# Optimization experiments

Hardware: AMD Instinct MI355X
Metric: run time of the kernel (lower is better)

The kernel has to match this reference:

```python
import jax, jax.numpy as jnp
import numpy as np

B, S, D, H = 4, 2048, 512, 8
DH = D // H  # depth per head = 64


def setup_inputs() -> dict:
    key = jax.random.key(0)
    ks = jax.random.split(key, 8)
    scale = 1.0 / np.sqrt(D)
    return {
        "query": jax.random.normal(ks[0], (B, S, D), jnp.float32),
        "key": jax.random.normal(ks[1], (B, S, D), jnp.float32),
        "value": jax.random.normal(ks[2], (B, S, D), jnp.float32),
        "mask": jax.random.randint(ks[3], (B, S), 0, 2, jnp.int32),
        "wq_w": jax.random.normal(ks[4], (D, D), jnp.float32) * scale,
        "wq_b": jnp.zeros((D,), jnp.float32),
        "wk_w": jax.random.normal(ks[5], (D, D), jnp.float32) * scale,
        "wk_b": jnp.zeros((D,), jnp.float32),
        "wv_w": jax.random.normal(ks[6], (D, D), jnp.float32) * scale,
        "wv_b": jnp.zeros((D,), jnp.float32),
        "wo_w": jax.random.normal(ks[7], (D, D), jnp.float32) * scale,
        "wo_b": jnp.zeros((D,), jnp.float32),
    }


def _split_heads(x):
    # [B, S, D] -> [B, H, S, DH]
    b, s, _ = x.shape
    return x.reshape(b, s, H, DH).transpose(0, 2, 1, 3)


def reference(query, key, value, mask, wq_w, wq_b, wk_w, wk_b, wv_w, wv_b, wo_w, wo_b):
    q = _split_heads(query @ wq_w + wq_b)   # [B,H,S,DH]
    k = _split_heads(key @ wk_w + wk_b)
    v = _split_heads(value @ wv_w + wv_b)

    scale = 1.0 / jnp.sqrt(jnp.asarray(DH, jnp.float32))
    logits = jnp.einsum('bhqd,bhkd->bhqk', q, k) * scale  # [B,H,S,S]
    # additive key-padding mask: 1 -> masked (adds -1e9)
    m = mask.astype(logits.dtype)[:, None, None, :]  # [B,1,1,S]
    logits = logits + m * -1e9
    weights = jax.nn.softmax(logits, axis=-1)
    attn = jnp.einsum('bhqk,bhkd->bhqd', weights, v)  # [B,H,S,DH]
    attn = attn.transpose(0, 2, 1, 3).reshape(query.shape[0], -1, D)  # [B,S,D]
    return attn @ wo_w + wo_b
```

## Files before the change

kernel.cpp:

```cpp
#include <hip/hip_runtime.h>
#include <stdint.h>

#define QSCALE (0.125f * 1.44269504088896340736f)
#define MASKNEG (-1.442695e9f)

typedef unsigned short u16;
typedef unsigned int u32;
typedef __bf16 bf16x8 __attribute__((ext_vector_type(8)));
typedef float f32x4 __attribute__((ext_vector_type(4)));
typedef float f32x16 __attribute__((ext_vector_type(16)));
typedef u16 u16x8 __attribute__((ext_vector_type(8)));
typedef u32 u32x4 __attribute__((ext_vector_type(4)));

__device__ __forceinline__ u16 f2bf(float f) {
  u32 u = __float_as_uint(f);
  u += 0x7fffu + ((u >> 16) & 1u);
  return (u16)(u >> 16);
}

__device__ __forceinline__ u32 cvtpk(float lo, float hi) {
  u32 d;
  asm("v_cvt_pk_bf16_f32 %0, %1, %2" : "=v"(d) : "v"(lo), "v"(hi));
  return d;
}

__device__ __forceinline__ void plswap(u32& a, u32& b) {
  asm("v_permlane32_swap_b32 %0, %1" : "+v"(a), "+v"(b));
}

__device__ __forceinline__ void gload16(const void* src, void* ldsbase) {
  __builtin_amdgcn_global_load_lds(
      (const __attribute__((address_space(1))) u32*)src,
      (__attribute__((address_space(3))) u32*)ldsbase, 16, 0, 0);
}

__device__ __forceinline__ u16x8 pack8(const float4& a, const float4& b) {
  u32x4 w;
  w[0] = cvtpk(a.x, a.y);
  w[1] = cvtpk(a.z, a.w);
  w[2] = cvtpk(b.x, b.y);
  w[3] = cvtpk(b.z, b.w);
  return __builtin_bit_cast(u16x8, w);
}

#define QKV_BAR(N)                                           \
  do {                                                       \
    asm volatile("s_waitcnt vmcnt(" #N ")" ::: "memory");    \
    asm volatile("s_waitcnt lgkmcnt(0)" ::: "memory");       \
    __builtin_amdgcn_sched_barrier(0);                       \
    __builtin_amdgcn_s_barrier();                            \
  } while (0)

__global__ __launch_bounds__(256) void conv_w(const float* __restrict__ wq,
                                              const float* __restrict__ wk,
                                              const float* __restrict__ wv,
                                              const float* __restrict__ wo,
                                              u16* __restrict__ wT) {
  const float* src = (blockIdx.z == 0) ? wq : (blockIdx.z == 1) ? wk
                    : (blockIdx.z == 2) ? wv : wo;
  u16* dst = wT + (size_t)blockIdx.z * 262144;
  __shared__ float t[64][65];
  const int n0 = blockIdx.x * 64, k0 = blockIdx.y * 64;
  const int lr = threadIdx.x >> 6, lc = threadIdx.x & 63;
#pragma unroll
  for (int it = 0; it < 16; ++it) {
    const int row = it * 4 + lr;
    t[row][lc] = src[(size_t)(k0 + row) * 512 + n0 + lc];
  }
  __syncthreads();
#pragma unroll
  for (int it = 0; it < 16; ++it) {
    const int row = it * 4 + lr;
    dst[(size_t)(n0 + row) * 512 + k0 + lc] = f2bf(t[lc][row]);
  }
}

__global__ __launch_bounds__(256, 2) void gemm_qkv(
    const float* __restrict__ xqf, const float* __restrict__ xkf,
    const float* __restrict__ xvf, const u16* __restrict__ wT,
    const float* __restrict__ bq, const float* __restrict__ bk,
    const float* __restrict__ bv, u16* __restrict__ qws, u16* __restrict__ kws,
    u16* __restrict__ vTw) {
  __shared__ __align__(16) char lds[65536];
  const int hw = blockIdx.x;
  const int lg = (hw & 7) * 96 + (hw >> 3);
  const int z = lg >> 8;
  const int rem = lg & 255;
  const int m0 = (rem >> 2) * 128, n0 = (rem & 3) * 128;
  const float* A = (z == 0) ? xqf : (z == 1) ? xkf : xvf;
  const u16* Bt = wT + (size_t)z * 262144;
  const float* bias = (z == 0) ? bq : (z == 1) ? bk : bv;

  const int tid = threadIdx.x;
  const int lane = tid & 63;
  const int wave = tid >> 6;
  const int wm = wave >> 1, wn = wave & 1;
  const int srow = tid >> 3;
  const int sc16 = tid & 7;

  f32x4 acc[4][4] = {};
  float4 s0[8], s1[8];

  auto stageB = [&](int buf, int kt) {
    const int k0 = kt * 64;
    char* base = lds + buf * 32768 + 16384;
#pragma unroll
    for (int c = 0; c < 4; ++c) {
      const int row = c * 32 + srow;
      const int xc = (sc16 ^ (row & 7)) << 3;
      gload16(Bt + (size_t)(n0 + row) * 512 + k0 + xc,
              base + c * 4096 + (wave << 10));
    }
  };

  auto loadA = [&](int kt, float4* ld) {
    const int k0 = kt * 64;
#pragma unroll
    for (int c = 0; c < 4; ++c) {
      const int row = c * 32 + srow;
      const float* sp = A + (size_t)(m0 + row) * 512 + k0 + sc16 * 8;
      ld[c * 2] = *(const float4*)sp;
      ld[c * 2 + 1] = *(const float4*)(sp + 4);
    }
  };

  auto writeA = [&](int buf, const float4* ld) {
    char* base = lds + buf * 32768;
#pragma unroll
    for (int c = 0; c < 4; ++c) {
      const int row = c * 32 + srow;
      *(u16x8*)(base + row * 128 + ((sc16 ^ (row & 7)) << 4)) =
          pack8(ld[c * 2], ld[c * 2 + 1]);
    }
  };

  auto compute = [&](int buf) {
    const char* bA = lds + buf * 32768;
    const char* bB = bA + 16384;
#pragma unroll
    for (int kk = 0; kk < 2; ++kk) {
      const int c16 = kk * 4 + (lane >> 4);
      bf16x8 av[4], bv[4];
#pragma unroll
      for (int i = 0; i < 4; ++i) {
        const int row = wm * 64 + i * 16 + (lane & 15);
        av[i] = *(const bf16x8*)(bA + row * 128 + ((c16 ^ (row & 7)) << 4));
      }
#pragma unroll
      for (int j = 0; j < 4; ++j) {
        const int row = wn * 64 + j * 16 + (lane & 15);
        bv[j] = *(const bf16x8*)(bB + row * 128 + ((c16 ^ (row & 7)) << 4));
      }
#pragma unroll
      for (int i = 0; i < 4; ++i)
#pragma unroll
        for (int j = 0; j < 4; ++j)
          acc[i][j] = __builtin_amdgcn_mfma_f32_16x16x32_bf16(av[i], bv[j],
                                                              acc[i][j], 0, 0, 0);
    }
  };

  stageB(0, 0);
  loadA(0, s0);
  loadA(1, s1);
  writeA(0, s0);
  QKV_BAR(8);

  stageB(1, 1); loadA(2, s0); writeA(1, s1); compute(0); QKV_BAR(8);
  stageB(0, 2); loadA(3, s1); writeA(0, s0); compute(1); QKV_BAR(8);
  stageB(1, 3); loadA(4, s0); writeA(1, s1); compute(0); QKV_BAR(8);
  stageB(0, 4); loadA(5, s1); writeA(0, s0); compute(1); QKV_BAR(8);
  stageB(1, 5); loadA(6, s0); writeA(1, s1); compute(0); QKV_BAR(8);
  stageB(0, 6); loadA(7, s1); writeA(0, s0); compute(1); QKV_BAR(8);
  stageB(1, 7);               writeA(1, s1); compute(0); QKV_BAR(0);
                                              compute(1);

#pragma unroll
  for (int j = 0; j < 4; ++j) {
    const int n = n0 + wn * 64 + j * 16 + (lane & 15);
    const float bn = bias[n];
    const int h = n >> 6, dh = n & 63;
#pragma unroll
    for (int i = 0; i < 4; ++i) {
#pragma unroll
      for (int r = 0; r < 4; ++r) {
        const int rg = m0 + wm * 64 + i * 16 + ((lane >> 4) << 2) + r;
        const int b = rg >> 11, s = rg & 2047;
        const int bh = b * 8 + h;
        const float val = acc[i][j][r] + bn;
        if (z == 0) {
          qws[((size_t)bh * 2048 + s) * 64 + dh] = f2bf(val * QSCALE);
        } else if (z == 1) {
          kws[((size_t)bh * 2048 + s) * 64 + dh] = f2bf(val);
        } else {
          vTw[((size_t)bh * 64 + dh) * 2048 + s] = f2bf(val);
        }
      }
    }
  }
}

__global__ __launch_bounds__(512, 4) void attn_fwd(
    const u16* __restrict__ qws, const u16* __restrict__ kws,
    const u16* __restrict__ vTw, const int* __restrict__ mask,
    u16* __restrict__ attn) {
  __shared__ __align__(16) char ldsK[32768];
  __shared__ __align__(16) char ldsV[32768];
  __shared__ __align__(16) float biasLDS[2048];
  __shared__ float lShA[128];

  const int bh = blockIdx.x;
  const int qt = blockIdx.y;
  const int b = bh >> 3;
  const int tid = threadIdx.x;
  const int lane = tid & 63, wave = tid >> 6;
  const int half = wave >> 2, wl = wave & 3;
  const int l31 = lane & 31, h5 = lane >> 5;

  {
    const int4 m4 = *(const int4*)(mask + b * 2048 + tid * 4);
    float4 bv;
    bv.x = m4.x ? MASKNEG : 0.0f;
    bv.y = m4.y ? MASKNEG : 0.0f;
    bv.z = m4.z ? MASKNEG : 0.0f;
    bv.w = m4.w ? MASKNEG : 0.0f;
    *(float4*)(biasLDS + tid * 4) = bv;
  }
  asm volatile("s_waitcnt lgkmcnt(0)" ::: "memory");

  const u16* qrow_p = qws + ((size_t)bh * 2048 + qt * 128 + wl * 32 + l31) * 64;
  bf16x8 qb[4];
#pragma unroll
  for (int c = 0; c < 4; ++c)
    qb[c] = *(const bf16x8*)(qrow_p + c * 16 + h5 * 8);

  const int rowb = l31 * 128;
  int kxs[4];
#pragma unroll
  for (int c = 0; c < 4; ++c) kxs[c] = ((2 * c + h5) ^ (l31 & 7)) << 4;

  char* myK = ldsK + half * 16384;
  char* myV = ldsV + half * 16384;
  const int srow = wl * 8 + (lane >> 3);
  const int sc16 = lane & 7;

  auto stage = [&](int buf, int ktg) {
#pragma unroll
    for (int c = 0; c < 2; ++c) {
      const int row = c * 32 + srow;
      const int xc = (sc16 ^ (row & 7)) << 3;
      gload16(kws + ((size_t)bh * 2048 + ktg * 64 + row) * 64 + xc,
              myK + buf * 8192 + c * 4096 + (wl << 10));
      gload16(vTw + ((size_t)bh * 64 + row) * 2048 + ktg * 64 + xc,
              myV + buf * 8192 + c * 4096 + (wl << 10));
    }
  };

  f32x16 o0 = {}, o1 = {};
  float rsp0 = 0.f, rsp1 = 0.f, rsp2 = 0.f, rsp3 = 0.f;

  auto do_subtile = [&](const char* kb, const char* vb, const float* biasT,
                        int stByte, int c0) {
    f32x16 sv;
#pragma unroll
    for (int g = 0; g < 4; ++g) {
      const f32x4 bq4 = *(const f32x4*)(biasT + g * 8 + h5 * 4);
      sv[g * 4 + 0] = bq4[0];
      sv[g * 4 + 1] = bq4[1];
      sv[g * 4 + 2] = bq4[2];
      sv[g * 4 + 3] = bq4[3];
    }
    __builtin_amdgcn_s_setprio(1);
#pragma unroll
    for (int c = 0; c < 4; ++c) {
      const bf16x8 kf = *(const bf16x8*)(kb + stByte + rowb + kxs[c]);
      sv = __builtin_amdgcn_mfma_f32_32x32x16_bf16(kf, qb[c], sv, 0, 0, 0);
    }
    __builtin_amdgcn_s_setprio(0);
    float p[16];
#pragma unroll
    for (int i = 0; i < 16; ++i) p[i] = __builtin_amdgcn_exp2f(sv[i]);
    rsp0 += p[0] + p[4] + p[8] + p[12];
    rsp1 += p[1] + p[5] + p[9] + p[13];
    rsp2 += p[2] + p[6] + p[10] + p[14];
    rsp3 += p[3] + p[7] + p[11] + p[15];
    u32 paw[2][4];
#pragma unroll
    for (int lc = 0; lc < 2; ++lc) {
      u32 a1 = cvtpk(p[lc * 8 + 0], p[lc * 8 + 1]);
      u32 b1 = cvtpk(p[lc * 8 + 4], p[lc * 8 + 5]);
      u32 a2 = cvtpk(p[lc * 8 + 2], p[lc * 8 + 3]);
      u32 b2 = cvtpk(p[lc * 8 + 6], p[lc * 8 + 7]);
      plswap(a1, b1);
      plswap(a2, b2);
      paw[lc][0] = a1; paw[lc][1] = a2; paw[lc][2] = b1; paw[lc][3] = b2;
    }
    __builtin_amdgcn_s_setprio(1);
#pragma unroll
    for (int lc = 0; lc < 2; ++lc) {
      u32x4 w = {paw[lc][0], paw[lc][1], paw[lc][2], paw[lc][3]};
      const bf16x8 pa = __builtin_bit_cast(bf16x8, w);
      const bf16x8 vf0 = *(const bf16x8*)(vb + rowb + kxs[c0 + lc]);
      o0 = __builtin_amdgcn_mfma_f32_32x32x16_bf16(pa, vf0, o0, 0, 0, 0);
      const bf16x8 vf1 = *(const bf16x8*)(vb + 4096 + rowb + kxs[c0 + lc]);
      o1 = __builtin_amdgcn_mfma_f32_32x32x16_bf16(pa, vf1, o1, 0, 0, 0);
    }
    __builtin_amdgcn_s_setprio(0);
  };

  stage(0, half * 16);

  for (int kt = 0; kt < 16; ++kt) {
    const int cur = kt & 1;
    const int ktg = half * 16 + kt;
    if (kt < 15) {
      stage(cur ^ 1, ktg + 1);
      asm volatile("s_waitcnt vmcnt(4)" ::: "memory");
    } else {
      asm volatile("s_waitcnt vmcnt(0)" ::: "memory");
    }
    __builtin_amdgcn_sched_barrier(0);
    __builtin_amdgcn_s_barrier();
    const char* kb = myK + cur * 8192;
    const char* vb = myV + cur * 8192;
    const float* biasT = biasLDS + ktg * 64;
    do_subtile(kb, vb, biasT, 0, 0);
    do_subtile(kb, vb, biasT + 32, 4096, 2);
    __builtin_amdgcn_sched_barrier(0);
    __builtin_amdgcn_s_barrier();
  }

  float rs = (rsp0 + rsp1) + (rsp2 + rsp3);
  rs += __shfl_xor(rs, 32);

  float* oSh2 = (float*)ldsK;
  u16* trb = (u16*)ldsV;
  if (half == 1) {
#pragma unroll
    for (int reg = 0; reg < 16; ++reg) {
      oSh2[(wl * 32 + reg) * 64 + lane] = o0[reg];
      oSh2[(wl * 32 + 16 + reg) * 64 + lane] = o1[reg];
    }
    if (h5 == 0) lShA[wl * 32 + l31] = rs;
  }
  __syncthreads();
  if (half == 0) {
    const float ltot = rs + lShA[wl * 32 + l31];
    const float linv = 1.0f / ltot;
#pragma unroll
    for (int reg = 0; reg < 16; ++reg) {
      const int q = (reg & 3) + 8 * (reg >> 2) + 4 * h5;
      const float inv = __shfl(linv, q);
      const float v0 = (o0[reg] + oSh2[(wl * 32 + reg) * 64 + lane]) * inv;
      const float v1 = (o1[reg] + oSh2[(wl * 32 + 16 + reg) * 64 + lane]) * inv;
      trb[(wl * 32 + q) * 64 + l31] = f2bf(v0);
      trb[(wl * 32 + q) * 64 + 32 + l31] = f2bf(v1);
    }
  }
  __syncthreads();
  const int h = bh & 7;
#pragma unroll
  for (int i = 0; i < 2; ++i) {
    const int ii = tid + i * 512;
    const int row = ii >> 3;
    const int c8 = (ii & 7) * 8;
    const u16x8 vv = *(const u16x8*)(trb + row * 64 + c8);
    const int grow = b * 2048 + qt * 128 + row;
    *(u16x8*)(attn + (size_t)grow * 512 + h * 64 + c8) = vv;
  }
}

__global__ __launch_bounds__(256, 3) void gemm_out(const u16* __restrict__ attn,
                                                   const u16* __restrict__ woT,
                                                   const float* __restrict__ bo,
                                                   float* __restrict__ out) {
  __shared__ __align__(16) char lds[49152];
  const int hw = blockIdx.x;
  const int lg = (hw & 7) * 64 + (hw >> 3);
  const int m0 = (lg >> 2) * 64, n0 = (lg & 3) * 128;

  const int tid = threadIdx.x;
  const int lane = tid & 63;
  const int wave = tid >> 6;
  const int wm = wave >> 1, wn = wave & 1;
  const int srow = tid >> 3;
  const int sc16 = tid & 7;

  f32x4 acc[2][4] = {};

  auto stage = [&](int buf, int kt) {
    const int k0 = kt * 64;
    char* base = lds + buf * 24576;
#pragma unroll
    for (int c = 0; c < 2; ++c) {
      const int row = c * 32 + srow;
      const int xc = (sc16 ^ (row & 7)) << 3;
      gload16(attn + (size_t)(m0 + row) * 512 + k0 + xc,
              base + c * 4096 + (wave << 10));
    }
#pragma unroll
    for (int c = 0; c < 4; ++c) {
      const int row = c * 32 + srow;
      const int xc = (sc16 ^ (row & 7)) << 3;
      gload16(woT + (size_t)(n0 + row) * 512 + k0 + xc,
              base + 8192 + c * 4096 + (wave << 10));
    }
  };

  auto compute = [&](int buf) {
    const char* bA = lds + buf * 24576;
    const char* bB = bA + 8192;
#pragma unroll
    for (int kk = 0; kk < 2; ++kk) {
      const int c16 = kk * 4 + (lane >> 4);
      bf16x8 av[2], bv[4];
#pragma unroll
      for (int i = 0; i < 2; ++i) {
        const int row = wm * 32 + i * 16 + (lane & 15);
        av[i] = *(const bf16x8*)(bA + row * 128 + ((c16 ^ (row & 7)) << 4));
      }
#pragma unroll
      for (int j = 0; j < 4; ++j) {
        const int row = wn * 64 + j * 16 + (lane & 15);
        bv[j] = *(const bf16x8*)(bB + row * 128 + ((c16 ^ (row & 7)) << 4));
      }
#pragma unroll
      for (int i = 0; i < 2; ++i)
#pragma unroll
        for (int j = 0; j < 4; ++j)
          acc[i][j] = __builtin_amdgcn_mfma_f32_16x16x32_bf16(av[i], bv[j],
                                                              acc[i][j], 0, 0, 0);
    }
  };

  stage(0, 0);
  __syncthreads();
#pragma unroll
  for (int kt = 0; kt < 8; ++kt) {
    const int cur = kt & 1;
    if (kt < 7) stage(cur ^ 1, kt + 1);
    compute(cur);
    __syncthreads();
  }

#pragma unroll
  for (int j = 0; j < 4; ++j) {
    const int n = n0 + wn * 64 + j * 16 + (lane & 15);
    const float bn = bo[n];
#pragma unroll
    for (int i = 0; i < 2; ++i) {
      const int rbase = m0 + wm * 32 + i * 16 + ((lane >> 4) << 2);
#pragma unroll
      for (int r = 0; r < 4; ++r)
        out[(size_t)(rbase + r) * 512 + n] = acc[i][j][r] + bn;
    }
  }
}

extern "C" void kernel_launch(void* const* d_in, const int* in_sizes, int n_in,
                              void* d_out, int out_size, void* d_ws,
                              size_t ws_size, hipStream_t stream) {
  (void)in_sizes; (void)n_in; (void)out_size; (void)ws_size;
  const float* q = (const float*)d_in[0];
  const float* k = (const float*)d_in[1];
  const float* v = (const float*)d_in[2];
  const int* mask = (const int*)d_in[3];
  const float* wq = (const float*)d_in[4];
  const float* bq = (const float*)d_in[5];
  const float* wk = (const float*)d_in[6];
  const float* bk = (const float*)d_in[7];
  const float* wv = (const float*)d_in[8];
  const float* bv = (const float*)d_in[9];
  const float* wo = (const float*)d_in[10];
  const float* bo = (const float*)d_in[11];

  u16* attnb = (u16*)d_ws;
  u16* wT = attnb + 4194304;
  u16* qws = wT + 1048576;
  u16* kws = qws + 4194304;
  u16* vTw = kws + 4194304;
  float* out = (float*)d_out;

  conv_w<<<dim3(8, 8, 4), 256, 0, stream>>>(wq, wk, wv, wo, wT);
  gemm_qkv<<<768, 256, 0, stream>>>(q, k, v, wT, bq, bk, bv, qws, kws, vTw);
  attn_fwd<<<dim3(32, 16), 512, 0, stream>>>(qws, kws, vTw, mask, attnb);
  gemm_out<<<512, 256, 0, stream>>>(attnb, wT + 786432, bo, out);
}
```

Measured before the change: 101.2 us.

## Pre-convert Q/K/V inputs to bf16 and stage both GEMM operands via direct LDS loads

```diff
diff --git a/kernel.cpp b/kernel.cpp
--- a/kernel.cpp
+++ b/kernel.cpp
@@ -34,22 +34,34 @@
       (__attribute__((address_space(3))) u32*)ldsbase, 16, 0, 0);
 }
 
-__device__ __forceinline__ u16x8 pack8(const float4& a, const float4& b) {
-  u32x4 w;
-  w[0] = cvtpk(a.x, a.y);
-  w[1] = cvtpk(a.z, a.w);
-  w[2] = cvtpk(b.x, b.y);
-  w[3] = cvtpk(b.z, b.w);
-  return __builtin_bit_cast(u16x8, w);
-}
-
-#define QKV_BAR(N)                                           \
+#define BAR_VM(N)                                            \
   do {                                                       \
     asm volatile("s_waitcnt vmcnt(" #N ")" ::: "memory");    \
+    __builtin_amdgcn_sched_barrier(0);                       \
+    __builtin_amdgcn_s_barrier();                            \
+  } while (0)
+
+#define BAR_LGKM()                                           \
+  do {                                                       \
     asm volatile("s_waitcnt lgkmcnt(0)" ::: "memory");       \
     __builtin_amdgcn_sched_barrier(0);                       \
     __builtin_amdgcn_s_barrier();                            \
   } while (0)
+
+__global__ __launch_bounds__(256) void conv_in(const float* __restrict__ q,
+                                               const float* __restrict__ k,
+                                               const float* __restrict__ v,
+                                               u16* __restrict__ dst) {
+  const float* src = (blockIdx.z == 0) ? q : (blockIdx.z == 1) ? k : v;
+  u16* d = dst + (size_t)blockIdx.z * 4194304;
+  size_t i = ((size_t)blockIdx.x * 256 + threadIdx.x) * 8;
+  float4 a = *(const float4*)(src + i);
+  float4 b = *(const float4*)(src + i + 4);
+  u16x8 ov;
+  ov[0] = f2bf(a.x); ov[1] = f2bf(a.y); ov[2] = f2bf(a.z); ov[3] = f2bf(a.w);
+  ov[4] = f2bf(b.x); ov[5] = f2bf(b.y); ov[6] = f2bf(b.z); ov[7] = f2bf(b.w);
+  *(u16x8*)(d + i) = ov;
+}
 
 __global__ __launch_bounds__(256) void conv_w(const float* __restrict__ wq,
                                               const float* __restrict__ wk,
@@ -75,9 +87,9 @@
   }
 }
 
-__global__ __launch_bounds__(256, 2) void gemm_qkv(
-    const float* __restrict__ xqf, const float* __restrict__ xkf,
-    const float* __restrict__ xvf, const u16* __restrict__ wT,
+__global__ __launch_bounds__(256) void gemm_qkv(
+    const u16* __restrict__ xq, const u16* __restrict__ xk,
+    const u16* __restrict__ xv, const u16* __restrict__ wT,
     const float* __restrict__ bq, const float* __restrict__ bk,
     const float* __restrict__ bv, u16* __restrict__ qws, u16* __restrict__ kws,
     u16* __restrict__ vTw) {
@@ -87,7 +99,7 @@
   const int z = lg >> 8;
   const int rem = lg & 255;
   const int m0 = (rem >> 2) * 128, n0 = (rem & 3) * 128;
-  const float* A = (z == 0) ? xqf : (z == 1) ? xkf : xvf;
+  const u16* A = (z == 0) ? xq : (z == 1) ? xk : xv;
   const u16* Bt = wT + (size_t)z * 262144;
   const float* bias = (z == 0) ? bq : (z == 1) ? bk : bv;
 
@@ -99,38 +111,18 @@
   const int sc16 = tid & 7;
 
   f32x4 acc[4][4] = {};
-  float4 s0[8], s1[8];
-
-  auto stageB = [&](int buf, int kt) {
+
+  auto stage = [&](int buf, int kt) {
     const int k0 = kt * 64;
-    char* base = lds + buf * 32768 + 16384;
+    char* base = lds + buf * 32768;
 #pragma unroll
     for (int c = 0; c < 4; ++c) {
       const int row = c * 32 + srow;
       const int xc = (sc16 ^ (row & 7)) << 3;
+      gload16(A + (size_t)(m0 + row) * 512 + k0 + xc,
+              base + c * 4096 + (wave << 10));
       gload16(Bt + (size_t)(n0 + row) * 512 + k0 + xc,
-              base + c * 4096 + (wave << 10));
-    }
-  };
-
-  auto loadA = [&](int kt, float4* ld) {
-    const int k0 = kt * 64;
-#pragma unroll
-    for (int c = 0; c < 4; ++c) {
-      const int row = c * 32 + srow;
-      const float* sp = A + (size_t)(m0 + row) * 512 + k0 + sc16 * 8;
-      ld[c * 2] = *(const float4*)sp;
-      ld[c * 2 + 1] = *(const float4*)(sp + 4);
-    }
-  };
-
-  auto writeA = [&](int buf, const float4* ld) {
-    char* base = lds + buf * 32768;
-#pragma unroll
-    for (int c = 0; c < 4; ++c) {
-      const int row = c * 32 + srow;
-      *(u16x8*)(base + row * 128 + ((sc16 ^ (row & 7)) << 4)) =
-          pack8(ld[c * 2], ld[c * 2 + 1]);
+              base + 16384 + c * 4096 + (wave << 10));
     }
   };
 
@@ -160,20 +152,24 @@
     }
   };
 
-  stageB(0, 0);
-  loadA(0, s0);
-  loadA(1, s1);
-  writeA(0, s0);
-  QKV_BAR(8);
-
-  stageB(1, 1); loadA(2, s0); writeA(1, s1); compute(0); QKV_BAR(8);
-  stageB(0, 2); loadA(3, s1); writeA(0, s0); compute(1); QKV_BAR(8);
-  stageB(1, 3); loadA(4, s0); writeA(1, s1); compute(0); QKV_BAR(8);
-  stageB(0, 4); loadA(5, s1); writeA(0, s0); compute(1); QKV_BAR(8);
-  stageB(1, 5); loadA(6, s0); writeA(1, s1); compute(0); QKV_BAR(8);
-  stageB(0, 6); loadA(7, s1); writeA(0, s0); compute(1); QKV_BAR(8);
-  stageB(1, 7);               writeA(1, s1); compute(0); QKV_BAR(0);
-                                              compute(1);
+  stage(0, 0);
+  asm volatile("s_waitcnt vmcnt(0)" ::: "memory");
+  __builtin_amdgcn_sched_barrier(0);
+  __builtin_amdgcn_s_barrier();
+#pragma unroll
+  for (int kt = 0; kt < 8; ++kt) {
+    const int cur = kt & 1;
+    if (kt < 7) {
+      stage(cur ^ 1, kt + 1);
+      asm volatile("s_waitcnt vmcnt(8)" ::: "memory");
+    } else {
+      asm volatile("s_waitcnt vmcnt(0)" ::: "memory");
+    }
+    __builtin_amdgcn_sched_barrier(0);
+    __builtin_amdgcn_s_barrier();
+    compute(cur);
+    BAR_LGKM();
+  }
 
 #pragma unroll
   for (int j = 0; j < 4; ++j) {
@@ -434,13 +430,22 @@
   };
 
   stage(0, 0);
-  __syncthreads();
+  asm volatile("s_waitcnt vmcnt(0)" ::: "memory");
+  __builtin_amdgcn_sched_barrier(0);
+  __builtin_amdgcn_s_barrier();
 #pragma unroll
   for (int kt = 0; kt < 8; ++kt) {
     const int cur = kt & 1;
-    if (kt < 7) stage(cur ^ 1, kt + 1);
+    if (kt < 7) {
+      stage(cur ^ 1, kt + 1);
+      asm volatile("s_waitcnt vmcnt(6)" ::: "memory");
+    } else {
+      asm volatile("s_waitcnt vmcnt(0)" ::: "memory");
+    }
+    __builtin_amdgcn_sched_barrier(0);
+    __builtin_amdgcn_s_barrier();
     compute(cur);
-    __syncthreads();
+    BAR_LGKM();
   }
 
 #pragma unroll
@@ -474,15 +479,19 @@
   const float* wo = (const float*)d_in[10];
   const float* bo = (const float*)d_in[11];
 
-  u16* attnb = (u16*)d_ws;
-  u16* wT = attnb + 4194304;
+  u16* xq = (u16*)d_ws;
+  u16* xk = xq + 4194304;
+  u16* xv = xk + 4194304;
+  u16* wT = xv + 4194304;
   u16* qws = wT + 1048576;
   u16* kws = qws + 4194304;
   u16* vTw = kws + 4194304;
+  u16* attnb = xq;
   float* out = (float*)d_out;
 
+  conv_in<<<dim3(2048, 1, 3), 256, 0, stream>>>(q, k, v, xq);
   conv_w<<<dim3(8, 8, 4), 256, 0, stream>>>(wq, wk, wv, wo, wT);
-  gemm_qkv<<<768, 256, 0, stream>>>(q, k, v, wT, bq, bk, bv, qws, kws, vTw);
+  gemm_qkv<<<768, 256, 0, stream>>>(xq, xk, xv, wT, bq, bk, bv, qws, kws, vTw);
   attn_fwd<<<dim3(32, 16), 512, 0, stream>>>(qws, kws, vTw, mask, attnb);
   gemm_out<<<512, 256, 0, stream>>>(attnb, wT + 786432, bo, out);
 }
```

Measured after the change: 107.6 us. +6.3%, slower.

## Stage fp32 activations directly to LDS via async loads in QKV GEMM

Applied to the files above, without the earlier changes.

```diff
diff --git a/kernel.cpp b/kernel.cpp
--- a/kernel.cpp
+++ b/kernel.cpp
@@ -33,23 +33,6 @@
       (const __attribute__((address_space(1))) u32*)src,
       (__attribute__((address_space(3))) u32*)ldsbase, 16, 0, 0);
 }
-
-__device__ __forceinline__ u16x8 pack8(const float4& a, const float4& b) {
-  u32x4 w;
-  w[0] = cvtpk(a.x, a.y);
-  w[1] = cvtpk(a.z, a.w);
-  w[2] = cvtpk(b.x, b.y);
-  w[3] = cvtpk(b.z, b.w);
-  return __builtin_bit_cast(u16x8, w);
-}
-
-#define QKV_BAR(N)                                           \
-  do {                                                       \
-    asm volatile("s_waitcnt vmcnt(" #N ")" ::: "memory");    \
-    asm volatile("s_waitcnt lgkmcnt(0)" ::: "memory");       \
-    __builtin_amdgcn_sched_barrier(0);                       \
-    __builtin_amdgcn_s_barrier();                            \
-  } while (0)
 
 __global__ __launch_bounds__(256) void conv_w(const float* __restrict__ wq,
                                               const float* __restrict__ wk,
@@ -75,13 +58,13 @@
   }
 }
 
-__global__ __launch_bounds__(256, 2) void gemm_qkv(
+__global__ __launch_bounds__(256, 3) void gemm_qkv(
     const float* __restrict__ xqf, const float* __restrict__ xkf,
     const float* __restrict__ xvf, const u16* __restrict__ wT,
     const float* __restrict__ bq, const float* __restrict__ bk,
     const float* __restrict__ bv, u16* __restrict__ qws, u16* __restrict__ kws,
     u16* __restrict__ vTw) {
-  __shared__ __align__(16) char lds[65536];
+  __shared__ __align__(16) char lds[49152];
   const int hw = blockIdx.x;
   const int lg = (hw & 7) * 96 + (hw >> 3);
   const int z = lg >> 8;
@@ -95,96 +78,87 @@
   const int lane = tid & 63;
   const int wave = tid >> 6;
   const int wm = wave >> 1, wn = wave & 1;
-  const int srow = tid >> 3;
-  const int sc16 = tid & 7;
+  const int h4 = lane >> 4, l15 = lane & 15;
 
   f32x4 acc[4][4] = {};
-  float4 s0[8], s1[8];
-
-  auto stageB = [&](int buf, int kt) {
-    const int k0 = kt * 64;
-    char* base = lds + buf * 32768 + 16384;
-#pragma unroll
-    for (int c = 0; c < 4; ++c) {
-      const int row = c * 32 + srow;
-      const int xc = (sc16 ^ (row & 7)) << 3;
-      gload16(Bt + (size_t)(n0 + row) * 512 + k0 + xc,
-              base + c * 4096 + (wave << 10));
-    }
-  };
-
-  auto loadA = [&](int kt, float4* ld) {
-    const int k0 = kt * 64;
-#pragma unroll
-    for (int c = 0; c < 4; ++c) {
-      const int row = c * 32 + srow;
-      const float* sp = A + (size_t)(m0 + row) * 512 + k0 + sc16 * 8;
-      ld[c * 2] = *(const float4*)sp;
-      ld[c * 2 + 1] = *(const float4*)(sp + 4);
-    }
-  };
-
-  auto writeA = [&](int buf, const float4* ld) {
-    char* base = lds + buf * 32768;
-#pragma unroll
-    for (int c = 0; c < 4; ++c) {
-      const int row = c * 32 + srow;
-      *(u16x8*)(base + row * 128 + ((sc16 ^ (row & 7)) << 4)) =
-          pack8(ld[c * 2], ld[c * 2 + 1]);
+
+  auto stage = [&](int buf, int kt) {
+    const int k0 = kt * 32;
+    char* baseA = lds + buf * 24576;
+    char* baseB = baseA + 16384;
+    {
+      const int sxA = tid & 7;
+#pragma unroll
+      for (int c = 0; c < 4; ++c) {
+        const int row = c * 32 + (tid >> 3);
+        const int sx = sxA ^ (row & 7);
+        gload16(A + (size_t)(m0 + row) * 512 + k0 + sx * 4,
+                baseA + row * 128 + (sx << 4));
+      }
+    }
+    {
+      const int sxB = tid & 3;
+#pragma unroll
+      for (int c = 0; c < 2; ++c) {
+        const int row = c * 64 + (tid >> 2);
+        const int sx = sxB ^ (row & 3);
+        gload16(Bt + (size_t)(n0 + row) * 512 + k0 + sx * 8,
+                baseB + row * 64 + (sx << 4));
+      }
     }
   };
 
   auto compute = [&](int buf) {
-    const char* bA = lds + buf * 32768;
+    const char* bA = lds + buf * 24576;
     const char* bB = bA + 16384;
-#pragma unroll
-    for (int kk = 0; kk < 2; ++kk) {
-      const int c16 = kk * 4 + (lane >> 4);
-      bf16x8 av[4], bv[4];
-#pragma unroll
-      for (int i = 0; i < 4; ++i) {
-        const int row = wm * 64 + i * 16 + (lane & 15);
-        av[i] = *(const bf16x8*)(bA + row * 128 + ((c16 ^ (row & 7)) << 4));
-      }
-#pragma unroll
-      for (int j = 0; j < 4; ++j) {
-        const int row = wn * 64 + j * 16 + (lane & 15);
-        bv[j] = *(const bf16x8*)(bB + row * 128 + ((c16 ^ (row & 7)) << 4));
-      }
-#pragma unroll
-      for (int i = 0; i < 4; ++i)
-#pragma unroll
-        for (int j = 0; j < 4; ++j)
-          acc[i][j] = __builtin_amdgcn_mfma_f32_16x16x32_bf16(av[i], bv[j],
-                                                              acc[i][j], 0, 0, 0);
-    }
-  };
-
-  stageB(0, 0);
-  loadA(0, s0);
-  loadA(1, s1);
-  writeA(0, s0);
-  QKV_BAR(8);
-
-  stageB(1, 1); loadA(2, s0); writeA(1, s1); compute(0); QKV_BAR(8);
-  stageB(0, 2); loadA(3, s1); writeA(0, s0); compute(1); QKV_BAR(8);
-  stageB(1, 3); loadA(4, s0); writeA(1, s1); compute(0); QKV_BAR(8);
-  stageB(0, 4); loadA(5, s1); writeA(0, s0); compute(1); QKV_BAR(8);
-  stageB(1, 5); loadA(6, s0); writeA(1, s1); compute(0); QKV_BAR(8);
-  stageB(0, 6); loadA(7, s1); writeA(0, s0); compute(1); QKV_BAR(8);
-  stageB(1, 7);               writeA(1, s1); compute(0); QKV_BAR(0);
-                                              compute(1);
+    bf16x8 av[4], bv[4];
+#pragma unroll
+    for (int i = 0; i < 4; ++i) {
+      const int row = wm * 64 + i * 16 + l15;
+      const f32x4 lo =
+          *(const f32x4*)(bA + row * 128 + (((h4 * 2) ^ (row & 7)) << 4));
+      const f32x4 hi =
+          *(const f32x4*)(bA + row * 128 + (((h4 * 2 + 1) ^ (row & 7)) << 4));
+      u32x4 w;
+      w[0] = cvtpk(lo[0], lo[1]);
+      w[1] = cvtpk(lo[2], lo[3]);
+      w[2] = cvtpk(hi[0], hi[1]);
+      w[3] = cvtpk(hi[2], hi[3]);
+      av[i] = __builtin_bit_cast(bf16x8, w);
+    }
+#pragma unroll
+    for (int j = 0; j < 4; ++j) {
+      const int row = wn * 64 + j * 16 + l15;
+      bv[j] = *(const bf16x8*)(bB + row * 64 + ((h4 ^ (row & 3)) << 4));
+    }
+#pragma unroll
+    for (int i = 0; i < 4; ++i)
+#pragma unroll
+      for (int j = 0; j < 4; ++j)
+        acc[i][j] = __builtin_amdgcn_mfma_f32_16x16x32_bf16(av[i], bv[j],
+                                                            acc[i][j], 0, 0, 0);
+  };
+
+  stage(0, 0);
+  __syncthreads();
+#pragma unroll
+  for (int kt = 0; kt < 16; ++kt) {
+    const int cur = kt & 1;
+    if (kt < 15) stage(cur ^ 1, kt + 1);
+    compute(cur);
+    __syncthreads();
+  }
 
 #pragma unroll
   for (int j = 0; j < 4; ++j) {
-    const int n = n0 + wn * 64 + j * 16 + (lane & 15);
+    const int n = n0 + wn * 64 + j * 16 + l15;
     const float bn = bias[n];
     const int h = n >> 6, dh = n & 63;
 #pragma unroll
     for (int i = 0; i < 4; ++i) {
 #pragma unroll
       for (int r = 0; r < 4; ++r) {
-        const int rg = m0 + wm * 64 + i * 16 + ((lane >> 4) << 2) + r;
+        const int rg = m0 + wm * 64 + i * 16 + h4 * 4 + r;
         const int b = rg >> 11, s = rg & 2047;
         const int bh = b * 8 + h;
         const float val = acc[i][j][r] + bn;
```

After: 100.7 us, median of 2. About the same (-0.6%).
